# Performance work log

Hardware: AMD Instinct MI355X
Metric: run time of the kernel (lower is better)

## Reference

```python
import jax, jax.numpy as jnp
import numpy as np

N = 100000            # number of nodes
E = 1600000           # number of edges (avg degree 16)
D = 32                # embedding dim
MASK_DEPTH = 3        # cfg.mask_depth
PATH_PROB = 0.5       # cfg.path_prob
NUM_MASK_CAND = 1024  # cfg.num_mask_cand
EPS_NORM = 1e-12      # F.normalize eps


def setup_inputs() -> dict:
    key = jax.random.key(0)
    k1, k2 = jax.random.split(key)
    edge_index = jax.random.randint(k1, (2, E), 0, N)  # [2, E] (row, col) COO indices
    adj_values = jnp.ones((E,), dtype=jnp.float32)     # sparse values (binary adjacency)
    embeds = jax.random.normal(k2, (N, D), dtype=jnp.float32)
    return {"edge_index": edge_index, "adj_values": adj_values, "embeds": embeds}


def _spmm(rows, cols, vals, x):
    # out[i] = sum_{e: rows[e]==i} vals[e] * x[cols[e]]  -- irregular gather + scatter-add
    return jax.ops.segment_sum(x[cols] * vals[:, None], rows, num_segments=N)


def _l2_normalize(x):
    n = jnp.sqrt(jnp.sum(x * x, axis=-1, keepdims=True))
    return x / jnp.maximum(n, EPS_NORM)


def reference(edge_index, adj_values, embeds):
    rows, cols = edge_index[0], edge_index[1]
    vals = adj_values

    # order = row-sums of sparse adj, shape [N, 1]
    order = jax.ops.segment_sum(vals, rows, num_segments=N)[:, None]

    fst_emb = _spmm(rows, cols, vals, embeds) - embeds
    fst_num = order
    emb = [fst_emb]
    num = [fst_num]

    drop_key = jax.random.key(42)
    for i in range(MASK_DEPTH):
        # sparse_dropout with keep prob path_prob**(i+1); zeroing values == dropping edges in spmm
        keep_prob = PATH_PROB ** (i + 1)
        u = jax.random.uniform(jax.random.fold_in(drop_key, i), (E,))
        keep = jnp.floor(u + keep_prob)  # 1.0 with prob keep_prob, else 0.0
        vals = vals * keep               # dropout compounds across iterations

        emb.append(_spmm(rows, cols, vals, emb[-1]) - emb[-1] - order * emb[-1])
        num.append(_spmm(rows, cols, vals, num[-1]) - num[-1] - order)
        order = jax.ops.segment_sum(vals, rows, num_segments=N)[:, None]

    subgraph_embeds = sum(emb) / (sum(num) + 1e-8)
    subgraph_embeds = _l2_normalize(subgraph_embeds)
    embeds_n = _l2_normalize(embeds)

    scores = jnp.sum(subgraph_embeds * embeds_n, axis=-1)  # [N]
    # Gumbel noise: -log(-log(U))
    u = jax.random.uniform(jax.random.key(7), (N,))
    scores = scores + (-jnp.log(-jnp.log(u)))

    _, candidates = jax.lax.top_k(scores, NUM_MASK_CAND)
    return scores, candidates
```

## Files before the change

### kernel.cpp

```cpp
#include <hip/hip_runtime.h>
#include <stdint.h>
#include <stddef.h>

#define NN 100000
#define NE 1600000
#define DD 32
#define NCAND 1024
#define HSIZE 65536
#define SORTN 4096
#define NBUK ((NN + 255) / 256)
#define EPB 4096
#define BCAP 5120
#define BCAPL 4608

#define CAP1 832000
#define CAP2 432000
#define CAP3 240000

__host__ __device__ inline void tf2x32(uint32_t k0, uint32_t k1, uint32_t x0, uint32_t x1,
                                       uint32_t& o0, uint32_t& o1) {
  uint32_t ks2 = k0 ^ k1 ^ 0x1BD11BDAu;
  uint32_t v0 = x0 + k0, v1 = x1 + k1;
#define TFR(r) { v0 += v1; v1 = (v1 << (r)) | (v1 >> (32 - (r))); v1 ^= v0; }
  TFR(13) TFR(15) TFR(26) TFR(6)   v0 += k1;  v1 += ks2 + 1u;
  TFR(17) TFR(29) TFR(16) TFR(24)  v0 += ks2; v1 += k0 + 2u;
  TFR(13) TFR(15) TFR(26) TFR(6)   v0 += k0;  v1 += k1 + 3u;
  TFR(17) TFR(29) TFR(16) TFR(24)  v0 += k1;  v1 += ks2 + 4u;
  TFR(13) TFR(15) TFR(26) TFR(6)   v0 += ks2; v1 += k0 + 5u;
#undef TFR
  o0 = v0; o1 = v1;
}

__device__ __forceinline__ uint32_t jax_bits32(uint32_t k0, uint32_t k1, uint32_t i) {
  uint32_t o0, o1;
  tf2x32(k0, k1, 0u, i, o0, o1);
  return o0 ^ o1;
}

__device__ __forceinline__ float bits_to_uniform(uint32_t b) {
  return __fsub_rn(__uint_as_float((b >> 9) | 0x3f800000u), 1.0f);
}

__device__ __forceinline__ float pairwise32(const float* x) {
  float r[8];
#pragma unroll
  for (int j = 0; j < 8; ++j) r[j] = x[j];
#pragma unroll
  for (int b = 8; b < 32; b += 8)
#pragma unroll
    for (int j = 0; j < 8; ++j) r[j] = __fadd_rn(r[j], x[b + j]);
  float a01 = __fadd_rn(r[0], r[1]), a23 = __fadd_rn(r[2], r[3]);
  float a45 = __fadd_rn(r[4], r[5]), a67 = __fadd_rn(r[6], r[7]);
  return __fadd_rn(__fadd_rn(a01, a23), __fadd_rn(a45, a67));
}


__global__ __launch_bounds__(512) void kA2_bin(
    const int* __restrict__ rows, const int* __restrict__ cols,
    const float* __restrict__ adj,
    uint32_t k00, uint32_t k01, uint32_t k10, uint32_t k11,
    uint32_t k20, uint32_t k21,
    int* __restrict__ bucketCursor, int4* __restrict__ pkBin,
    int* __restrict__ bucketCntS) {
  __shared__ int hist[NBUK];
  __shared__ int base[NBUK];
  __shared__ int h1[NBUK];
  __shared__ int h2[NBUK];
  __shared__ int h3[NBUK];
  __shared__ uint8_t lvs[EPB];
  __shared__ uint16_t rank16[EPB];
  int tid = threadIdx.x;
  for (int i = tid; i < NBUK; i += 512) { hist[i] = 0; h1[i] = 0; h2[i] = 0; h3[i] = 0; }
  __syncthreads();
  int e0 = blockIdx.x * EPB;
  for (int k = 0; k < 8; ++k) {
    int e = e0 + k * 512 + tid;
    int lv = 0;
    if (e < NE) {
      float u0 = bits_to_uniform(jax_bits32(k00, k01, (uint32_t)e));
      float u1 = bits_to_uniform(jax_bits32(k10, k11, (uint32_t)e));
      float u2 = bits_to_uniform(jax_bits32(k20, k21, (uint32_t)e));
      float kp0 = floorf(__fadd_rn(u0, 0.5f));
      float kp1 = floorf(__fadd_rn(u1, 0.25f));
      float kp2 = floorf(__fadd_rn(u2, 0.125f));
      if (kp0 != 0.0f) { lv = 1; if (kp1 != 0.0f) { lv = 2; if (kp2 != 0.0f) lv = 3; } }
      int b = rows[e] >> 8;
      rank16[k * 512 + tid] = (uint16_t)atomicAdd(&hist[b], 1);
      if (lv >= 1) {
        atomicAdd(&h1[b], 1);
        if (lv >= 2) {
          atomicAdd(&h2[b], 1);
          if (lv >= 3) atomicAdd(&h3[b], 1);
        }
      }
    }
    lvs[k * 512 + tid] = (uint8_t)lv;
  }
  __syncthreads();
  for (int i = tid; i < NBUK; i += 512) {
    int h = hist[i];
    base[i] = (h > 0) ? atomicAdd(&bucketCursor[i], h) : 0;
    if (h) atomicAdd(&bucketCntS[i], h);
    if (h1[i]) atomicAdd(&bucketCntS[NBUK + i], h1[i]);
    if (h2[i]) atomicAdd(&bucketCntS[2 * NBUK + i], h2[i]);
    if (h3[i]) atomicAdd(&bucketCntS[3 * NBUK + i], h3[i]);
  }
  __syncthreads();
  for (int k = 0; k < 8; ++k) {
    int e = e0 + k * 512 + tid;
    if (e < NE) {
      int r = rows[e];
      int b = r >> 8;
      int lv = (int)lvs[k * 512 + tid];
      int pos = base[b] + (int)rank16[k * 512 + tid];
      if (pos < BCAP)
        pkBin[(size_t)b * BCAP + pos] =
            make_int4(cols[e], __float_as_int(adj[e]), (e << 2) | lv, r);
    }
  }
}

__global__ __launch_bounds__(512) void k_scanBS(const int* __restrict__ bucketCntS,
                                                int* __restrict__ bucketBaseS) {
  __shared__ int sb[512];
  int a = blockIdx.x;
  const int* c = bucketCntS + (size_t)a * NBUK;
  int* o = bucketBaseS + (size_t)a * (NBUK + 1);
  int tid = threadIdx.x;
  int v = (tid < NBUK) ? c[tid] : 0;
  sb[tid] = v;
  __syncthreads();
  for (int off = 1; off < 512; off <<= 1) {
    int x = (tid >= off) ? sb[tid - off] : 0;
    __syncthreads();
    sb[tid] += x;
    __syncthreads();
  }
  if (tid < NBUK) o[tid] = sb[tid] - v;
  if (tid == NBUK - 1) o[NBUK] = sb[tid];
}

__global__ __launch_bounds__(512) void kB_emit(
    const int* __restrict__ bucketBaseS, const int4* __restrict__ pkBin,
    int* __restrict__ rpAll,
    int2* __restrict__ pk0, int2* __restrict__ pk1,
    int2* __restrict__ pk2, int2* __restrict__ pk3,
    float* __restrict__ order0, float* __restrict__ order1, float* __restrict__ order2) {
  __shared__ unsigned long long cnt64[256];
  __shared__ unsigned long long scan64[512];
  __shared__ int start0[256];
  __shared__ int cur[256];
  __shared__ uint32_t keyF[BCAPL];
  __shared__ uint32_t keyG[BCAPL];
  __shared__ uint16_t origG[BCAPL];
  int b = blockIdx.x, tid = threadIdx.x;
  int bB0 = bucketBaseS[b];
  int n = bucketBaseS[b + 1] - bB0;
  if (n > BCAPL) n = BCAPL;
  size_t sRead = (size_t)b * BCAP;
  const int* pkI = (const int*)pkBin;
  const int2* pkZW = (const int2*)pkBin;
  int r0 = b << 8;
  int nr = NN - r0; if (nr > 256) nr = 256;
  int bB1 = bucketBaseS[(NBUK + 1) + b];
  int bB2 = bucketBaseS[2 * (NBUK + 1) + b];
  int bB3 = bucketBaseS[3 * (NBUK + 1) + b];
  if (tid < 256) { cnt64[tid] = 0ull; cur[tid] = 0; }
  __syncthreads();
  for (int i = tid; i < n; i += 512) {
    int2 zw = pkZW[2 * (sRead + (size_t)i) + 1];
    int lr = zw.y - r0;
    int lv = zw.x & 3;
    keyF[i] = ((uint32_t)lr << 23) | (uint32_t)zw.x;
    unsigned long long add = 1ull;
    if (lv >= 1) add |= 1ull << 16;
    if (lv >= 2) add |= 1ull << 32;
    if (lv >= 3) add |= 1ull << 48;
    atomicAdd(&cnt64[lr], add);
  }
  __syncthreads();
  unsigned long long own = (tid < 256) ? cnt64[tid] : 0ull;
  if (tid < 256) scan64[tid] = own;
  __syncthreads();
  for (int off = 1; off < 256; off <<= 1) {
    unsigned long long v = (tid < 256 && tid >= off) ? scan64[tid - off] : 0ull;
    __syncthreads();
    if (tid < 256) scan64[tid] += v;
    __syncthreads();
  }
  if (tid < 256) {
    unsigned long long ex = scan64[tid] - own;
    start0[tid] = (int)(ex & 0xFFFFull);
    if (tid < nr) {
      rpAll[r0 + tid] = bB0 + (int)(ex & 0xFFFFull);
      rpAll[(NN + 1) + r0 + tid] = bB1 + (int)((ex >> 16) & 0xFFFFull);
      rpAll[2 * (NN + 1) + r0 + tid] = bB2 + (int)((ex >> 32) & 0xFFFFull);
      rpAll[3 * (NN + 1) + r0 + tid] = bB3 + (int)((ex >> 48) & 0xFFFFull);
    }
  }
  if (b == NBUK - 1 && tid == 0) {
    rpAll[NN] = bucketBaseS[NBUK];
    rpAll[(NN + 1) + NN] = bucketBaseS[(NBUK + 1) + NBUK];
    rpAll[2 * (NN + 1) + NN] = bucketBaseS[2 * (NBUK + 1) + NBUK];
    rpAll[3 * (NN + 1) + NN] = bucketBaseS[3 * (NBUK + 1) + NBUK];
  }
  __syncthreads();
  for (int i = tid; i < n; i += 512) {
    uint32_t k = keyF[i];
    int lr = (int)(k >> 23);
    int slot = start0[lr] + atomicAdd(&cur[lr], 1);
    origG[slot] = (uint16_t)i;
    keyG[slot] = k;
  }
  __syncthreads();
  int C2 = (n + 511) >> 9;
  {
    int lo2 = tid * C2, hi2 = lo2 + C2;
    if (lo2 > n) lo2 = n;
    if (hi2 > n) hi2 = n;
    uint16_t vals[10];
    uint16_t pos[10];
    uint32_t keys[10];
#pragma unroll
    for (int q = 0; q < 10; ++q) {
      int i = lo2 + q;
      if (i < hi2) {
        uint32_t ki = keyG[i];
        int lr = (int)(ki >> 23);
        int st = start0[lr];
        int d = (int)(cnt64[lr] & 0xFFFFull);
        int rank = 0;
        for (int j = 0; j < d; ++j) rank += (keyG[st + j] < ki) ? 1 : 0;
        vals[q] = origG[i];
        keys[q] = ki;
        pos[q] = (uint16_t)(st + rank);
      }
    }
    __syncthreads();
#pragma unroll
    for (int q = 0; q < 10; ++q) {
      int i = lo2 + q;
      if (i < hi2) { origG[pos[q]] = vals[q]; keyG[pos[q]] = keys[q]; }
    }
  }
  __syncthreads();
  uint32_t* adjS = keyF;
  {
    uint32_t av[10];
#pragma unroll
    for (int q = 0; q < 10; ++q) {
      int i = tid + q * 512;
      if (i < n) av[q] = (uint32_t)pkI[4 * (sRead + (size_t)origG[i]) + 1];
    }
#pragma unroll
    for (int q = 0; q < 10; ++q) {
      int i = tid + q * 512;
      if (i < n) adjS[i] = av[q];
    }
  }
  __syncthreads();
  if (tid < nr) {
    int d = (int)(cnt64[tid] & 0xFFFFull);
    int st = start0[tid];
    float o0 = 0.0f, o1v = 0.0f, o2v = 0.0f;
    for (int i = 0; i < d; ++i) {
      int lv = (int)(keyG[st + i] & 3u);
      float a = __uint_as_float(adjS[st + i]);
      o0 = __fadd_rn(o0, a);
      if (lv >= 1) { o1v = __fadd_rn(o1v, a); if (lv >= 2) o2v = __fadd_rn(o2v, a); }
    }
    order0[r0 + tid] = o0; order1[r0 + tid] = o1v; order2[r0 + tid] = o2v;
  }
  int lo = tid * C2, hi = lo + C2;
  if (lo > n) lo = n;
  if (hi > n) hi = n;
  int c1 = 0, c2 = 0, c3 = 0;
  for (int i = lo; i < hi; ++i) {
    int lv = (int)(keyG[i] & 3u);
    c1 += (lv >= 1); c2 += (lv >= 2); c3 += (lv >= 3);
  }
  unsigned long long mine = (unsigned long long)c1 |
                            ((unsigned long long)c2 << 16) |
                            ((unsigned long long)c3 << 32);
  scan64[tid] = mine;
  __syncthreads();
  for (int off = 1; off < 512; off <<= 1) {
    unsigned long long v = (tid >= off) ? scan64[tid - off] : 0ull;
    __syncthreads();
    scan64[tid] += v;
    __syncthreads();
  }
  unsigned long long ex = scan64[tid] - mine;
  int o1 = bB1 + (int)(ex & 0xFFFFull);
  int o2 = bB2 + (int)((ex >> 16) & 0xFFFFull);
  int o3 = bB3 + (int)((ex >> 32) & 0xFFFFull);
  {
    int colr[10];
#pragma unroll
    for (int q = 0; q < 10; ++q) {
      int i = lo + q;
      if (i < hi) colr[q] = pkI[4 * (sRead + (size_t)origG[i])];
    }
#pragma unroll
    for (int q = 0; q < 10; ++q) {
      int i = lo + q;
      if (i < hi) {
        int lv = (int)(keyG[i] & 3u);
        int2 pkv = make_int2(colr[q], (int)adjS[i]);
        pk0[bB0 + i] = pkv;
        if (lv >= 1) {
          pk1[o1++] = pkv;
          if (lv >= 2) {
            pk2[o2++] = pkv;
            if (lv >= 3) pk3[o3++] = pkv;
          }
        }
      }
    }
  }
}


__global__ void k_emb0(const int* __restrict__ rp, const int2* __restrict__ pk,
                       const float* __restrict__ embeds, float* __restrict__ e0) {
  int tid = blockIdx.x * blockDim.x + threadIdx.x;
  int r = tid >> 5, d = tid & 31;
  if (r >= NN) return;
  int s = rp[r], t = rp[r + 1];
  float acc = 0.0f;
  for (int base = s; base < t; base += 32) {
    int idx = base + d;
    int2 p = (idx < t) ? pk[idx] : make_int2(0, 0);
    int m = t - base; if (m > 32) m = 32;
    for (int j = 0; j < m; j += 8) {
      int cc[8], aa[8];
      float xx[8];
#pragma unroll
      for (int q = 0; q < 8; ++q) {
        cc[q] = __shfl(p.x, j + q, 32);
        aa[q] = __shfl(p.y, j + q, 32);
      }
#pragma unroll
      for (int q = 0; q < 8; ++q) xx[q] = embeds[(size_t)cc[q] * DD + d];
#pragma unroll
      for (int q = 0; q < 8; ++q)
        acc = __fadd_rn(acc, __fmul_rn(__int_as_float(aa[q]), xx[q]));
    }
  }
  e0[(size_t)r * DD + d] = __fsub_rn(acc, embeds[(size_t)r * DD + d]);
}

__global__ void k_emb_step(const int* __restrict__ rp, const int2* __restrict__ pk,
                           const float* __restrict__ ord, const float* __restrict__ ecur,
                           float* __restrict__ enext, float* __restrict__ esum,
                           const float* __restrict__ ncur, float* __restrict__ nnext,
                           float* __restrict__ nsum, int mode) {
  int tid = blockIdx.x * blockDim.x + threadIdx.x;
  int r = tid >> 5, d = tid & 31;
  if (r >= NN) return;
  int s = rp[r], t = rp[r + 1];
  float acc = 0.0f, accn = 0.0f;
  for (int base = s; base < t; base += 32) {
    int idx = base + d;
    int2 p = (idx < t) ? pk[idx] : make_int2(0, 0);
    int m = t - base; if (m > 32) m = 32;
    for (int j = 0; j < m; j += 8) {
      int cc[8], aa[8];
      float xx[8], nn[8];
#pragma unroll
      for (int q = 0; q < 8; ++q) {
        cc[q] = __shfl(p.x, j + q, 32);
        aa[q] = __shfl(p.y, j + q, 32);
      }
#pragma unroll
      for (int q = 0; q < 8; ++q) {
        xx[q] = ecur[(size_t)cc[q] * DD + d];
        nn[q] = ncur[cc[q]];
      }
#pragma unroll
      for (int q = 0; q < 8; ++q) {
        float av = __int_as_float(aa[q]);
        acc = __fadd_rn(acc, __fmul_rn(av, xx[q]));
        accn = __fadd_rn(accn, __fmul_rn(av, nn[q]));
      }
    }
  }
  float ordv = ord[r];
  size_t idx = (size_t)r * DD + d;
  float ec = ecur[idx];
  float o = __fsub_rn(__fsub_rn(acc, ec), __fmul_rn(ordv, ec));
  if (mode != 3) enext[idx] = o;
  if (mode == 1) esum[idx] = __fadd_rn(ec, o);
  else esum[idx] = __fadd_rn(esum[idx], o);
  if (d == 0) {
    float nc = ncur[r];
    float on = __fsub_rn(__fsub_rn(accn, nc), ordv);
    if (mode != 3) nnext[r] = on;
    if (mode == 1) nsum[r] = __fadd_rn(nc, on);
    else nsum[r] = __fadd_rn(nsum[r], on);
  }
}

__global__ __launch_bounds__(256) void k_final(
    const float* __restrict__ embeds, const float* __restrict__ emb_sum,
    const float* __restrict__ num_sum, uint32_t gk0, uint32_t gk1,
    float* __restrict__ out_scores, int* __restrict__ hist) {
  __shared__ uint32_t hb[512];
  __shared__ uint32_t hc[512];
  int r = blockIdx.x * blockDim.x + threadIdx.x;
  for (int i = threadIdx.x; i < 512; i += 256) { hb[i] = 0xFFFFFFFFu; hc[i] = 0u; }
  __syncthreads();
  if (r < NN) {
    float denom = __fadd_rn(num_sum[r], 1e-8f);
    float sub[DD], em[DD], pr[DD];
    const float4* ps = (const float4*)(emb_sum + (size_t)r * DD);
    const float4* pe = (const float4*)(embeds + (size_t)r * DD);
#pragma unroll
    for (int j = 0; j < 8; ++j) {
      float4 a = ps[j], b = pe[j];
      sub[4 * j + 0] = __fdiv_rn(a.x, denom); sub[4 * j + 1] = __fdiv_rn(a.y, denom);
      sub[4 * j + 2] = __fdiv_rn(a.z, denom); sub[4 * j + 3] = __fdiv_rn(a.w, denom);
      em[4 * j + 0] = b.x; em[4 * j + 1] = b.y; em[4 * j + 2] = b.z; em[4 * j + 3] = b.w;
    }
#pragma unroll
    for (int d = 0; d < DD; ++d) pr[d] = __fmul_rn(sub[d], sub[d]);
    float n1 = fmaxf(__fsqrt_rn(pairwise32(pr)), 1e-12f);
#pragma unroll
    for (int d = 0; d < DD; ++d) pr[d] = __fmul_rn(em[d], em[d]);
    float n2 = fmaxf(__fsqrt_rn(pairwise32(pr)), 1e-12f);
#pragma unroll
    for (int d = 0; d < DD; ++d)
      pr[d] = __fmul_rn(__fdiv_rn(sub[d], n1), __fdiv_rn(em[d], n2));
    float dot = pairwise32(pr);
    float u = bits_to_uniform(jax_bits32(gk0, gk1, (uint32_t)r));
    float l1 = (float)log((double)u);
    float w = -l1;
    float l2 = (float)log((double)w);
    float g = -l2;
    float score = __fadd_rn(dot, g);
    out_scores[r] = score;
    uint32_t kb = __float_as_uint(score);
    kb = (kb & 0x80000000u) ? ~kb : (kb | 0x80000000u);
    uint32_t key = kb >> 16;
    uint32_t slot = (key * 2654435761u) >> 23;
    for (;;) {
      uint32_t prev = atomicCAS(&hb[slot], 0xFFFFFFFFu, key);
      if (prev == 0xFFFFFFFFu || prev == key) { atomicAdd(&hc[slot], 1u); break; }
      slot = (slot + 1) & 511u;
    }
  }
  __syncthreads();
  for (int i = threadIdx.x; i < 512; i += 256)
    if (hb[i] != 0xFFFFFFFFu) atomicAdd(&hist[hb[i]], (int)hc[i]);
}

__global__ void k_cutoff(const int* __restrict__ hist, int* __restrict__ cutoff) {
  __shared__ int psum[1024];
  int t = threadIdx.x;
  int base = HSIZE - (t + 1) * 64;
  int own = 0;
  for (int i = 0; i < 64; ++i) own += hist[base + i];
  psum[t] = own;
  __syncthreads();
  for (int off = 1; off < 1024; off <<= 1) {
    int v = (t >= off) ? psum[t - off] : 0;
    __syncthreads();
    psum[t] += v;
    __syncthreads();
  }
  int incl = psum[t];
  int prev = incl - own;
  if (incl >= NCAND && prev < NCAND) {
    int c = prev;
    int b = HSIZE - t * 64 - 1;
    while (b >= base) {
      c += hist[b];
      if (c >= NCAND) break;
      --b;
    }
    *cutoff = b;
  }
}

__global__ void k_collect(const float* __restrict__ scores, const int* __restrict__ cutoff,
                          unsigned long long* __restrict__ buf, int* __restrict__ cnt2) {
  int r = blockIdx.x * blockDim.x + threadIdx.x;
  if (r >= NN) return;
  uint32_t kb = __float_as_uint(scores[r]);
  kb = (kb & 0x80000000u) ? ~kb : (kb | 0x80000000u);
  if ((int)(kb >> 16) >= *cutoff) {
    int p = atomicAdd(cnt2, 1);
    if (p < SORTN)
      buf[p] = ((unsigned long long)kb << 32) | (uint32_t)(~(uint32_t)r);
  }
}

__global__ __launch_bounds__(256) void k_rank(const unsigned long long* __restrict__ buf,
                                              const int* __restrict__ cnt2,
                                              float* __restrict__ out_cand) {
  __shared__ unsigned long long s[SORTN];
  int m = *cnt2;
  if (m > SORTN) m = SORTN;
  if (blockIdx.x * 256 >= m) return;
  for (int i = threadIdx.x; i < m; i += 256) s[i] = buf[i];
  __syncthreads();
  int i = blockIdx.x * 256 + threadIdx.x;
  if (i >= m) return;
  unsigned long long mine = s[i];
  int rank = 0;
  int j = 0;
  for (; j + 8 <= m; j += 8) {
#pragma unroll
    for (int q = 0; q < 8; ++q) rank += (s[j + q] > mine) ? 1 : 0;
  }
  for (; j < m; ++j) rank += (s[j] > mine) ? 1 : 0;
  if (rank < NCAND) {
    uint32_t idx = ~((uint32_t)(mine & 0xffffffffull));
    out_cand[rank] = (float)idx;
  }
}

extern "C" void kernel_launch(void* const* d_in, const int* in_sizes, int n_in,
                              void* d_out, int out_size, void* d_ws, size_t ws_size,
                              hipStream_t stream) {
  const int* rows = (const int*)d_in[0];
  const int* cols = rows + NE;
  const float* adj = (const float*)d_in[1];
  const float* embeds = (const float*)d_in[2];
  float* out = (float*)d_out;

  char* p = (char*)d_ws;
  auto alloc = [&](size_t bytes) {
    char* q = p;
    p += (bytes + 255) & ~(size_t)255;
    return q;
  };
  size_t zero_bytes = (size_t)(5 * NBUK + HSIZE + 8) * 4;
  char* zero_base = (char*)alloc(zero_bytes);
  int* bucketCursor = (int*)zero_base;
  int* bucketCntS = bucketCursor + NBUK;
  int* hist = bucketCntS + 4 * NBUK;
  int* cnt2 = hist + HSIZE;

  int* bucketBaseS = (int*)alloc((size_t)4 * (NBUK + 1) * 4);
  int* rpAll = (int*)alloc((size_t)4 * (NN + 1) * 4);
  size_t padBytes = (size_t)NBUK * BCAP * 16;
  char* unionAB = (char*)alloc(padBytes);
  int4* pkBin = (int4*)unionAB;
  float* embA = (float*)unionAB;
  float* embB = (float*)(unionAB + (size_t)NN * DD * 4);
  int2* pk0 = (int2*)alloc((size_t)NE * 8);
  int2* pk1 = (int2*)alloc((size_t)CAP1 * 8);
  int2* pk2 = (int2*)alloc((size_t)CAP2 * 8);
  int2* pk3 = (int2*)alloc((size_t)CAP3 * 8);
  float* embS = (float*)alloc((size_t)NN * DD * 4);
  float* order0 = (float*)alloc(NN * 4);
  float* order1 = (float*)alloc(NN * 4);
  float* order2 = (float*)alloc(NN * 4);
  float* num1 = (float*)alloc(NN * 4);
  float* num2 = (float*)alloc(NN * 4);
  float* numS = (float*)alloc(NN * 4);
  unsigned long long* buf = (unsigned long long*)alloc(SORTN * 8);

  uint32_t dk[3][2];
  for (int i = 0; i < 3; ++i) tf2x32(0u, 42u, 0u, (uint32_t)i, dk[i][0], dk[i][1]);

  hipMemsetAsync(zero_base, 0, zero_bytes, stream);

  int gE = (NE + EPB - 1) / EPB;
  kA2_bin<<<gE, 512, 0, stream>>>(rows, cols, adj, dk[0][0], dk[0][1], dk[1][0], dk[1][1],
                                  dk[2][0], dk[2][1], bucketCursor, pkBin, bucketCntS);
  k_scanBS<<<4, 512, 0, stream>>>(bucketCntS, bucketBaseS);
  kB_emit<<<NBUK, 512, 0, stream>>>(bucketBaseS, pkBin, rpAll,
                                    pk0, pk1, pk2, pk3, order0, order1, order2);

  const int* rp0 = rpAll;
  const int* rp1 = rpAll + (NN + 1);
  const int* rp2 = rpAll + 2 * (NN + 1);
  const int* rp3 = rpAll + 3 * (NN + 1);

  int gEmb = (NN * 32 + 255) / 256;
  k_emb0<<<gEmb, 256, 0, stream>>>(rp0, pk0, embeds, embA);

  k_emb_step<<<gEmb, 256, 0, stream>>>(rp1, pk1, order0, embA, embB, embS,
                                       order0, num1, numS, 1);
  k_emb_step<<<gEmb, 256, 0, stream>>>(rp2, pk2, order1, embB, embA, embS,
                                       num1, num2, numS, 2);
  k_emb_step<<<gEmb, 256, 0, stream>>>(rp3, pk3, order2, embA, embB, embS,
                                       num2, num1, numS, 3);

  k_final<<<(NN + 255) / 256, 256, 0, stream>>>(embeds, embS, numS, 0u, 7u, out, hist);
  k_cutoff<<<1, 1024, 0, stream>>>(hist, cnt2 + 1);
  k_collect<<<(NN + 255) / 256, 256, 0, stream>>>(out, cnt2 + 1, buf, cnt2);
  k_rank<<<(SORTN + 255) / 256, 256, 0, stream>>>(buf, cnt2, out + NN);
}
```

Measured before the change: 339.6 us.

## Split edge binning into RNG/histogram, per-bucket scan, and deterministic scatter passes

The single binning kernel is replaced by three passes. The first generates the dropout levels and packs four per-bucket counters into one shared atomic per edge. The second runs a per-bucket prefix scan over the per-block histograms, and the third scatters edges to deterministic offsets. This removes the global atomics on bucket cursors and count arrays, the workspace memset of those arrays, and the float uniform conversion. In exchange it adds two extra launches, a scratch packed array of per-edge metadata and a 1024-thread scan per bucket, and it relies on packed counter fields not overflowing at EPB=2048.

```diff
diff --git a/kernel.cpp b/kernel.cpp
--- a/kernel.cpp
+++ b/kernel.cpp
@@ -9,7 +9,8 @@
 #define HSIZE 65536
 #define SORTN 4096
 #define NBUK ((NN + 255) / 256)
-#define EPB 4096
+#define EPB 2048
+#define NBLK ((NE + EPB - 1) / EPB)
 #define BCAP 5120
 #define BCAPL 4608
 
@@ -55,67 +56,94 @@
 }
 
 
-__global__ __launch_bounds__(512) void kA2_bin(
-    const int* __restrict__ rows, const int* __restrict__ cols,
-    const float* __restrict__ adj,
+__global__ __launch_bounds__(512) void kA2a_rng(
+    const int* __restrict__ rows,
     uint32_t k00, uint32_t k01, uint32_t k10, uint32_t k11,
     uint32_t k20, uint32_t k21,
-    int* __restrict__ bucketCursor, int4* __restrict__ pkBin,
-    int* __restrict__ bucketCntS) {
-  __shared__ int hist[NBUK];
-  __shared__ int base[NBUK];
-  __shared__ int h1[NBUK];
-  __shared__ int h2[NBUK];
-  __shared__ int h3[NBUK];
-  __shared__ uint8_t lvs[EPB];
-  __shared__ uint16_t rank16[EPB];
+    uint32_t* __restrict__ packArr, uint32_t* __restrict__ histGB) {
+  __shared__ uint32_t cnt[NBUK];
   int tid = threadIdx.x;
-  for (int i = tid; i < NBUK; i += 512) { hist[i] = 0; h1[i] = 0; h2[i] = 0; h3[i] = 0; }
+  for (int i = tid; i < NBUK; i += 512) cnt[i] = 0u;
   __syncthreads();
   int e0 = blockIdx.x * EPB;
-  for (int k = 0; k < 8; ++k) {
-    int e = e0 + k * 512 + tid;
-    int lv = 0;
-    if (e < NE) {
-      float u0 = bits_to_uniform(jax_bits32(k00, k01, (uint32_t)e));
-      float u1 = bits_to_uniform(jax_bits32(k10, k11, (uint32_t)e));
-      float u2 = bits_to_uniform(jax_bits32(k20, k21, (uint32_t)e));
-      float kp0 = floorf(__fadd_rn(u0, 0.5f));
-      float kp1 = floorf(__fadd_rn(u1, 0.25f));
-      float kp2 = floorf(__fadd_rn(u2, 0.125f));
-      if (kp0 != 0.0f) { lv = 1; if (kp1 != 0.0f) { lv = 2; if (kp2 != 0.0f) lv = 3; } }
-      int b = rows[e] >> 8;
-      rank16[k * 512 + tid] = (uint16_t)atomicAdd(&hist[b], 1);
-      if (lv >= 1) {
-        atomicAdd(&h1[b], 1);
-        if (lv >= 2) {
-          atomicAdd(&h2[b], 1);
-          if (lv >= 3) atomicAdd(&h3[b], 1);
-        }
-      }
-    }
-    lvs[k * 512 + tid] = (uint8_t)lv;
-  }
-  __syncthreads();
-  for (int i = tid; i < NBUK; i += 512) {
-    int h = hist[i];
-    base[i] = (h > 0) ? atomicAdd(&bucketCursor[i], h) : 0;
-    if (h) atomicAdd(&bucketCntS[i], h);
-    if (h1[i]) atomicAdd(&bucketCntS[NBUK + i], h1[i]);
-    if (h2[i]) atomicAdd(&bucketCntS[2 * NBUK + i], h2[i]);
-    if (h3[i]) atomicAdd(&bucketCntS[3 * NBUK + i], h3[i]);
-  }
-  __syncthreads();
-  for (int k = 0; k < 8; ++k) {
+#pragma unroll
+  for (int k = 0; k < 4; ++k) {
     int e = e0 + k * 512 + tid;
     if (e < NE) {
+      uint32_t b0 = jax_bits32(k00, k01, (uint32_t)e);
+      uint32_t b1 = jax_bits32(k10, k11, (uint32_t)e);
+      uint32_t b2 = jax_bits32(k20, k21, (uint32_t)e);
+      int lv = 0;
+      if (b0 >= 0x80000000u) {
+        lv = 1;
+        if (b1 >= 0xC0000000u) { lv = 2; if (b2 >= 0xE0000000u) lv = 3; }
+      }
       int r = rows[e];
       int b = r >> 8;
-      int lv = (int)lvs[k * 512 + tid];
-      int pos = base[b] + (int)rank16[k * 512 + tid];
+      uint32_t enc = 1u;
+      if (lv >= 1) { enc += 1u << 10; if (lv >= 2) { enc += 1u << 18; if (lv >= 3) enc += 1u << 25; } }
+      uint32_t old = atomicAdd(&cnt[b], enc);
+      uint32_t rank = old & 1023u;
+      packArr[e] = ((uint32_t)b << 23) | ((uint32_t)(r & 255) << 15) |
+                   ((uint32_t)lv << 13) | rank;
+    }
+  }
+  __syncthreads();
+  for (int i = tid; i < NBUK; i += 512)
+    histGB[(size_t)blockIdx.x * NBUK + i] = cnt[i];
+}
+
+__global__ __launch_bounds__(1024) void kT_scan(
+    const uint32_t* __restrict__ histGB, uint32_t* __restrict__ relBase,
+    int* __restrict__ bucketCntS) {
+  __shared__ unsigned long long s64[1024];
+  int b = blockIdx.x;
+  int g = threadIdx.x;
+  uint32_t h = (g < NBLK) ? histGB[(size_t)g * NBUK + b] : 0u;
+  unsigned long long v = (unsigned long long)(h & 1023u)
+    | ((unsigned long long)((h >> 10) & 255u) << 16)
+    | ((unsigned long long)((h >> 18) & 127u) << 32)
+    | ((unsigned long long)((h >> 25) & 127u) << 48);
+  s64[g] = v;
+  __syncthreads();
+  for (int off = 1; off < 1024; off <<= 1) {
+    unsigned long long x = (g >= off) ? s64[g - off] : 0ull;
+    __syncthreads();
+    s64[g] += x;
+    __syncthreads();
+  }
+  if (g < NBLK) relBase[(size_t)g * NBUK + b] = (uint32_t)((s64[g] - v) & 0xFFFFull);
+  if (g == NBLK - 1) {
+    unsigned long long inc = s64[g];
+    bucketCntS[b] = (int)(inc & 0xFFFFull);
+    bucketCntS[NBUK + b] = (int)((inc >> 16) & 0xFFFFull);
+    bucketCntS[2 * NBUK + b] = (int)((inc >> 32) & 0xFFFFull);
+    bucketCntS[3 * NBUK + b] = (int)((inc >> 48) & 0xFFFFull);
+  }
+}
+
+__global__ __launch_bounds__(512) void kA2b_bin(
+    const int* __restrict__ cols, const float* __restrict__ adj,
+    const uint32_t* __restrict__ packArr, const uint32_t* __restrict__ relBase,
+    int4* __restrict__ pkBin) {
+  __shared__ uint32_t rb[NBUK];
+  int g = blockIdx.x, tid = threadIdx.x;
+  for (int i = tid; i < NBUK; i += 512) rb[i] = relBase[(size_t)g * NBUK + i];
+  __syncthreads();
+  int e0 = g * EPB;
+#pragma unroll
+  for (int k = 0; k < 4; ++k) {
+    int e = e0 + k * 512 + tid;
+    if (e < NE) {
+      uint32_t pv = packArr[e];
+      int b = (int)(pv >> 23);
+      int lr = (int)((pv >> 15) & 255u);
+      int lv = (int)((pv >> 13) & 3u);
+      int rank = (int)(pv & 0x1FFFu);
+      int pos = (int)rb[b] + rank;
       if (pos < BCAP)
         pkBin[(size_t)b * BCAP + pos] =
-            make_int4(cols[e], __float_as_int(adj[e]), (e << 2) | lv, r);
+            make_int4(cols[e], __float_as_int(adj[e]), (e << 2) | lv, (b << 8) | lr);
     }
   }
 }
@@ -535,15 +563,17 @@
     p += (bytes + 255) & ~(size_t)255;
     return q;
   };
-  size_t zero_bytes = (size_t)(5 * NBUK + HSIZE + 8) * 4;
+  size_t zero_bytes = (size_t)(HSIZE + 8) * 4;
   char* zero_base = (char*)alloc(zero_bytes);
-  int* bucketCursor = (int*)zero_base;
-  int* bucketCntS = bucketCursor + NBUK;
-  int* hist = bucketCntS + 4 * NBUK;
+  int* hist = (int*)zero_base;
   int* cnt2 = hist + HSIZE;
 
+  int* bucketCntS = (int*)alloc((size_t)4 * NBUK * 4);
   int* bucketBaseS = (int*)alloc((size_t)4 * (NBUK + 1) * 4);
   int* rpAll = (int*)alloc((size_t)4 * (NN + 1) * 4);
+  uint32_t* packArr = (uint32_t*)alloc((size_t)NE * 4);
+  uint32_t* histGB = (uint32_t*)alloc((size_t)NBLK * NBUK * 4);
+  uint32_t* relBase = (uint32_t*)alloc((size_t)NBLK * NBUK * 4);
   size_t padBytes = (size_t)NBUK * BCAP * 16;
   char* unionAB = (char*)alloc(padBytes);
   int4* pkBin = (int4*)unionAB;
@@ -567,9 +597,10 @@
 
   hipMemsetAsync(zero_base, 0, zero_bytes, stream);
 
-  int gE = (NE + EPB - 1) / EPB;
-  kA2_bin<<<gE, 512, 0, stream>>>(rows, cols, adj, dk[0][0], dk[0][1], dk[1][0], dk[1][1],
-                                  dk[2][0], dk[2][1], bucketCursor, pkBin, bucketCntS);
+  kA2a_rng<<<NBLK, 512, 0, stream>>>(rows, dk[0][0], dk[0][1], dk[1][0], dk[1][1],
+                                     dk[2][0], dk[2][1], packArr, histGB);
+  kT_scan<<<NBUK, 1024, 0, stream>>>(histGB, relBase, bucketCntS);
+  kA2b_bin<<<NBLK, 512, 0, stream>>>(cols, adj, packArr, relBase, pkBin);
   k_scanBS<<<4, 512, 0, stream>>>(bucketCntS, bucketBaseS);
   kB_emit<<<NBUK, 512, 0, stream>>>(bucketBaseS, pkBin, rpAll,
                                     pk0, pk1, pk2, pk3, order0, order1, order2);
```

Measured after the change: 346.5 us. 2.0% more time.
